# Kernel tuning notes

Hardware: AMD Instinct MI355X
Metric: run time of the kernel (lower is better)

Reference implementation:

```python
import jax, jax.numpy as jnp
import numpy as np

N_NODES = 100000
N_EDGES = 3200000
IN_CH, HID_CH, OUT_CH = 128, 64, 40


def gcn_conv(x, row, col, norm, W, b, n_nodes):
    # linear transform first (PyG GCNConv order), then normalized aggregation
    h = x @ W                                   # [N, out]
    msg = h[row] * norm[:, None]                # [E+N, out] gathered & scaled
    out = jax.ops.segment_sum(msg, col, num_segments=n_nodes)
    return out + b


def setup_inputs() -> dict:
    key = jax.random.key(0)
    k0, k1, k2, k3, k4, k5 = jax.random.split(key, 6)
    x = jax.random.normal(k0, (N_NODES, IN_CH), dtype=jnp.float32)
    edge_index = jax.random.randint(k1, (2, N_EDGES), 0, N_NODES, dtype=jnp.int64)
    # Glorot-ish init for weights
    W1 = jax.random.normal(k2, (IN_CH, HID_CH), dtype=jnp.float32) * (1.0 / np.sqrt(IN_CH))
    b1 = jnp.zeros((HID_CH,), dtype=jnp.float32)
    W2 = jax.random.normal(k3, (HID_CH, OUT_CH), dtype=jnp.float32) * (1.0 / np.sqrt(HID_CH))
    b2 = jnp.zeros((OUT_CH,), dtype=jnp.float32)
    return {"x": x, "edge_index": edge_index, "original_size": N_NODES,
            "W1": W1, "b1": b1, "W2": W2, "b2": b2}


def reference(x, edge_index, original_size, W1, b1, W2, b2):
    n = x.shape[0]
    # add self-loops (GCNConv default)
    loops = jnp.arange(n, dtype=edge_index.dtype)
    row = jnp.concatenate([edge_index[0], loops])   # source
    col = jnp.concatenate([edge_index[1], loops])   # target
    # symmetric normalization: deg over targets with unit edge weights
    deg = jax.ops.segment_sum(jnp.ones_like(col, dtype=x.dtype), col, num_segments=n)
    dinv = jnp.where(deg > 0, jax.lax.rsqrt(deg), 0.0)
    norm = dinv[row] * dinv[col]                    # [E+N]
    h = gcn_conv(x, row, col, norm, W1, b1, n)
    h = gcn_conv(h, row, col, norm, W2, b2, n)
    out = jax.nn.log_softmax(h, axis=1)
    return out[:original_size]
```

## Files before the change

### kernel.cpp

```cpp
#include <hip/hip_runtime.h>
#include <math.h>


#define NN 100000
#define NE 3200000
#define NBUK 391
#define BCAP 8704
#define EPB 16384
#define NBB ((NE + EPB - 1) / EPB)
#define NGB 782

typedef __attribute__((ext_vector_type(2))) float f32x2;


__device__ __forceinline__ unsigned bf16rne(float x) {
  unsigned u = __float_as_uint(x);
  return (u + 0x7fffu + ((u >> 16) & 1u)) >> 16;
}
__device__ __forceinline__ unsigned pack2(float lo, float hi) {
  return bf16rne(lo) | (bf16rne(hi) << 16);
}


__device__ __forceinline__ void pkfma(f32x2& a, f32x2 v, f32x2 f) {
  asm("v_pk_fma_f32 %0, %1, %2, %0" : "+v"(a) : "v"(v), "v"(f));
}

#define ACCP(vv, fp) {                                                      \
  f32x2 t0, t1, t2, t3;                                                     \
  t0.x = __uint_as_float((vv).x << 16);                                     \
  t0.y = __uint_as_float((vv).x & 0xffff0000u);                             \
  t1.x = __uint_as_float((vv).y << 16);                                     \
  t1.y = __uint_as_float((vv).y & 0xffff0000u);                             \
  t2.x = __uint_as_float((vv).z << 16);                                     \
  t2.y = __uint_as_float((vv).z & 0xffff0000u);                             \
  t3.x = __uint_as_float((vv).w << 16);                                     \
  t3.y = __uint_as_float((vv).w & 0xffff0000u);                             \
  pkfma(acc2[0], t0, fp);                                                   \
  pkfma(acc2[1], t1, fp);                                                   \
  pkfma(acc2[2], t2, fp);                                                   \
  pkfma(acc2[3], t3, fp);                                                   \
}


__global__ __launch_bounds__(256) void k_bucket_gemm1(const int* __restrict__ ei,
                                                      int* __restrict__ tail,
                                                      unsigned* __restrict__ bucket,
                                                      const float* __restrict__ x,
                                                      const float* __restrict__ W1,
                                                      unsigned* __restrict__ m1b) {
  __shared__ float smem[128 * 64 + 16 * 132];
  const int tid = threadIdx.x;
  const int bx = blockIdx.x;

  if (bx < NBB) {
    int* hist  = (int*)smem;
    int* wbase = hist + NBUK;
    int* loc   = wbase + NBUK;
    const int beg = bx * EPB;
    const int end = min(beg + EPB, NE);
    const int* col = ei + NE;
    for (int b = tid; b < NBUK; b += 256) { hist[b] = 0; loc[b] = 0; }
    __syncthreads();
    for (int e = beg + tid * 4; e < end; e += 1024) {
      int4 c4 = *(const int4*)(col + e);
      atomicAdd(&hist[c4.x >> 8], 1);
      atomicAdd(&hist[c4.y >> 8], 1);
      atomicAdd(&hist[c4.z >> 8], 1);
      atomicAdd(&hist[c4.w >> 8], 1);
    }
    __syncthreads();
    for (int b = tid; b < NBUK; b += 256)
      wbase[b] = atomicAdd(&tail[b], hist[b]);
    __syncthreads();
    for (int e = beg + tid * 4; e < end; e += 1024) {
      int4 c4 = *(const int4*)(col + e);
      int4 r4 = *(const int4*)(ei + e);
      {
        int b = c4.x >> 8;
        unsigned pos = (unsigned)(wbase[b] + atomicAdd(&loc[b], 1));
        if (pos < BCAP) bucket[(size_t)b * BCAP + pos] = ((unsigned)r4.x << 8) | (unsigned)(c4.x & 255);
      }
      {
        int b = c4.y >> 8;
        unsigned pos = (unsigned)(wbase[b] + atomicAdd(&loc[b], 1));
        if (pos < BCAP) bucket[(size_t)b * BCAP + pos] = ((unsigned)r4.y << 8) | (unsigned)(c4.y & 255);
      }
      {
        int b = c4.z >> 8;
        unsigned pos = (unsigned)(wbase[b] + atomicAdd(&loc[b], 1));
        if (pos < BCAP) bucket[(size_t)b * BCAP + pos] = ((unsigned)r4.z << 8) | (unsigned)(c4.z & 255);
      }
      {
        int b = c4.w >> 8;
        unsigned pos = (unsigned)(wbase[b] + atomicAdd(&loc[b], 1));
        if (pos < BCAP) bucket[(size_t)b * BCAP + pos] = ((unsigned)r4.w << 8) | (unsigned)(c4.w & 255);
      }
    }
    return;
  }

  float* ws = smem;
  float* xt = smem + 128 * 64;
  const int row0 = (bx - NBB) * 128;
  {
    const float4* __restrict__ w4 = (const float4*)W1;
    float4* __restrict__ s4 = (float4*)ws;
    for (int i = tid; i < 128 * 16; i += 256) s4[i] = w4[i];
  }
  const int cg = tid & 7;
  const int rg = tid >> 3;
  const int srow = tid & 127;
  const int skh = tid >> 7;
  float acc[4][8];
  #pragma unroll
  for (int i = 0; i < 4; ++i)
    #pragma unroll
    for (int j = 0; j < 8; ++j) acc[i][j] = 0.f;
  const float4* __restrict__ xt4 = (const float4*)xt;
  const float4* __restrict__ ws4 = (const float4*)ws;
  for (int ks = 0; ks < 8; ++ks) {
    __syncthreads();
    {
      int grow = row0 + srow; if (grow > NN - 1) grow = NN - 1;
      const float* xp = x + (size_t)grow * 128 + ks * 16 + skh * 8;
      float4 va = *(const float4*)xp;
      float4 vb = *(const float4*)(xp + 4);
      const int kb = skh * 8;
      xt[(kb + 0) * 132 + srow] = va.x;
      xt[(kb + 1) * 132 + srow] = va.y;
      xt[(kb + 2) * 132 + srow] = va.z;
      xt[(kb + 3) * 132 + srow] = va.w;
      xt[(kb + 4) * 132 + srow] = vb.x;
      xt[(kb + 5) * 132 + srow] = vb.y;
      xt[(kb + 6) * 132 + srow] = vb.z;
      xt[(kb + 7) * 132 + srow] = vb.w;
    }
    __syncthreads();
    #pragma unroll 4
    for (int kk = 0; kk < 16; ++kk) {
      const int k = ks * 16 + kk;
      float4 xv = xt4[kk * 33 + rg];
      float4 wa = ws4[k * 16 + cg * 2];
      float4 wb = ws4[k * 16 + cg * 2 + 1];
      float xr[4] = {xv.x, xv.y, xv.z, xv.w};
      float wc[8] = {wa.x, wa.y, wa.z, wa.w, wb.x, wb.y, wb.z, wb.w};
      #pragma unroll
      for (int i = 0; i < 4; ++i)
        #pragma unroll
        for (int j = 0; j < 8; ++j)
          acc[i][j] = fmaf(xr[i], wc[j], acc[i][j]);
    }
  }
  #pragma unroll
  for (int i = 0; i < 4; ++i) {
    const int row = row0 + rg * 4 + i;
    if (row < NN) {
      uint4 o;
      o.x = pack2(acc[i][0], acc[i][1]);
      o.y = pack2(acc[i][2], acc[i][3]);
      o.z = pack2(acc[i][4], acc[i][5]);
      o.w = pack2(acc[i][6], acc[i][7]);
      ((uint4*)m1b)[row * 8 + cg] = o;
    }
  }
}


__global__ __launch_bounds__(256) void k_sort(const unsigned* __restrict__ bucket,
                                              const int* __restrict__ tail,
                                              int* __restrict__ csr_src,
                                              int* __restrict__ offsets,
                                              float* __restrict__ dinv,
                                              unsigned* __restrict__ m1b) {
  __shared__ int h[256], base_[256], loc[256];
  __shared__ float dv[256];
  __shared__ int sorted[BCAP];
  __shared__ int wsum[4];
  __shared__ int seg0_s;
  const int b = blockIdx.x;
  const int lo = b << 8;
  const int nc = min(256, NN - lo);
  const int n = min(tail[b], BCAP);
  const unsigned* __restrict__ bk = bucket + (size_t)b * BCAP;
  const int tid = threadIdx.x, lane = tid & 63, wid = tid >> 6;
  h[tid] = 0; loc[tid] = 0;
  if (wid == 0) {
    int local = 0;
    const int lim = (b < NBUK) ? b : NBUK;
    for (int j = lane; j < lim; j += 64) local += min(tail[j], BCAP);
    #pragma unroll
    for (int d = 32; d > 0; d >>= 1) local += __shfl_xor(local, d, 64);
    if (lane == 0) seg0_s = local;
  }
  __syncthreads();
  const int seg0 = seg0_s;
  int i = tid * 4;
  for (; i + 3 < n; i += 1024) {
    uint4 v = *(const uint4*)(bk + i);
    atomicAdd(&h[v.x & 255u], 1);
    atomicAdd(&h[v.y & 255u], 1);
    atomicAdd(&h[v.z & 255u], 1);
    atomicAdd(&h[v.w & 255u], 1);
  }
  for (; i < n; ++i) atomicAdd(&h[bk[i] & 255u], 1);
  __syncthreads();
  {
    int v = h[tid];
    int s = v;
    #pragma unroll
    for (int d = 1; d < 64; d <<= 1) { int t = __shfl_up(s, d, 64); if (lane >= d) s += t; }
    if (lane == 63) wsum[wid] = s;
    __syncthreads();
    int wpre = 0;
    #pragma unroll
    for (int w = 0; w < 4; ++w) if (w < wid) wpre += wsum[w];
    int excl = wpre + s - v;
    base_[tid] = excl;
    const float dval = rsqrtf((float)(v + 1));
    dv[tid] = dval;
    if (tid < nc) {
      dinv[lo + tid] = dval;
      offsets[lo + tid] = seg0 + excl;
    }
  }
  if (b == NBUK - 1 && tid == 0) offsets[NN] = seg0 + n;
  __syncthreads();
  i = tid * 4;
  for (; i + 3 < n; i += 1024) {
    uint4 v = *(const uint4*)(bk + i);
    { int c = v.x & 255u; sorted[base_[c] + atomicAdd(&loc[c], 1)] = (int)(v.x >> 8); }
    { int c = v.y & 255u; sorted[base_[c] + atomicAdd(&loc[c], 1)] = (int)(v.y >> 8); }
    { int c = v.z & 255u; sorted[base_[c] + atomicAdd(&loc[c], 1)] = (int)(v.z >> 8); }
    { int c = v.w & 255u; sorted[base_[c] + atomicAdd(&loc[c], 1)] = (int)(v.w >> 8); }
  }
  for (; i < n; ++i) {
    unsigned ent = bk[i];
    int c = ent & 255u;
    sorted[base_[c] + atomicAdd(&loc[c], 1)] = (int)(ent >> 8);
  }
  __syncthreads();
  for (int t = tid; t < n; t += 256) csr_src[seg0 + t] = sorted[t];
  {
    const int q = tid & 7;
    uint4* __restrict__ m1rw = (uint4*)m1b;
    for (int r = tid >> 3; r < nc; r += 32) {
      const float d = dv[r];
      uint4 v = m1rw[(size_t)(lo + r) * 8 + q];
      v.x = pack2(__uint_as_float(v.x << 16) * d, __uint_as_float(v.x & 0xffff0000u) * d);
      v.y = pack2(__uint_as_float(v.y << 16) * d, __uint_as_float(v.y & 0xffff0000u) * d);
      v.z = pack2(__uint_as_float(v.z << 16) * d, __uint_as_float(v.z & 0xffff0000u) * d);
      v.w = pack2(__uint_as_float(v.w << 16) * d, __uint_as_float(v.w & 0xffff0000u) * d);
      m1rw[(size_t)(lo + r) * 8 + q] = v;
    }
  }
}


__global__ __launch_bounds__(256) void k_agg1(const unsigned* __restrict__ m1b,
                                              const int* __restrict__ offsets,
                                              const int* __restrict__ csr_src,
                                              const float* __restrict__ dinv,
                                              const float* __restrict__ b1,
                                              float* __restrict__ a1) {
  const int node = blockIdx.x * 4 + (threadIdx.x >> 6);
  const int lane = threadIdx.x & 63;
  const int e = lane >> 3;
  const int q = lane & 7;
  const uint4* __restrict__ m1v = (const uint4*)m1b;
  const int beg = offsets[node], end = offsets[node + 1];
  f32x2 acc2[4];
  #pragma unroll
  for (int j = 0; j < 4; ++j) { acc2[j].x = 0.f; acc2[j].y = 0.f; }
  for (int p = beg; p < end; p += 32) {
    const int i0 = p + e, i1 = p + 8 + e, i2 = p + 16 + e, i3 = p + 24 + e;
    const int s0 = csr_src[i0 < end ? i0 : beg];
    const int s1 = csr_src[i1 < end ? i1 : beg];
    const int s2 = csr_src[i2 < end ? i2 : beg];
    const int s3 = csr_src[i3 < end ? i3 : beg];
    f32x2 f0; f0.x = f0.y = (i0 < end) ? 1.f : 0.f;
    f32x2 f1; f1.x = f1.y = (i1 < end) ? 1.f : 0.f;
    f32x2 f2; f2.x = f2.y = (i2 < end) ? 1.f : 0.f;
    f32x2 f3; f3.x = f3.y = (i3 < end) ? 1.f : 0.f;
    uint4 v0 = m1v[s0 * 8 + q];
    uint4 v1 = m1v[s1 * 8 + q];
    uint4 v2 = m1v[s2 * 8 + q];
    uint4 v3 = m1v[s3 * 8 + q];
    ACCP(v0, f0);
    ACCP(v1, f1);
    ACCP(v2, f2);
    ACCP(v3, f3);
  }
  float acc[8];
  acc[0] = acc2[0].x; acc[1] = acc2[0].y; acc[2] = acc2[1].x; acc[3] = acc2[1].y;
  acc[4] = acc2[2].x; acc[5] = acc2[2].y; acc[6] = acc2[3].x; acc[7] = acc2[3].y;
  #pragma unroll
  for (int j = 0; j < 8; ++j) {
    acc[j] += __shfl_xor(acc[j], 8, 64);
    acc[j] += __shfl_xor(acc[j], 16, 64);
    acc[j] += __shfl_xor(acc[j], 32, 64);
  }
  if (e == 0) {
    uint4 sv = m1v[node * 8 + q];
    const float d = dinv[node];
    float4 bb0 = ((const float4*)b1)[q * 2];
    float4 bb1 = ((const float4*)b1)[q * 2 + 1];
    float4 o0, o1;
    o0.x = (acc[0] + __uint_as_float(sv.x << 16)) * d + bb0.x;
    o0.y = (acc[1] + __uint_as_float(sv.x & 0xffff0000u)) * d + bb0.y;
    o0.z = (acc[2] + __uint_as_float(sv.y << 16)) * d + bb0.z;
    o0.w = (acc[3] + __uint_as_float(sv.y & 0xffff0000u)) * d + bb0.w;
    o1.x = (acc[4] + __uint_as_float(sv.z << 16)) * d + bb1.x;
    o1.y = (acc[5] + __uint_as_float(sv.z & 0xffff0000u)) * d + bb1.y;
    o1.z = (acc[6] + __uint_as_float(sv.w << 16)) * d + bb1.z;
    o1.w = (acc[7] + __uint_as_float(sv.w & 0xffff0000u)) * d + bb1.w;
    ((float4*)a1)[node * 16 + q * 2] = o0;
    ((float4*)a1)[node * 16 + q * 2 + 1] = o1;
  }
}


__global__ __launch_bounds__(256) void k_gemm2(const float* __restrict__ a1,
                                               const float* __restrict__ W2,
                                               const float* __restrict__ dinv,
                                               unsigned* __restrict__ m2b) {
  __shared__ float ws[64 * 40];
  const int tid = threadIdx.x;
  for (int k = tid; k < 64 * 40; k += 256) ws[k] = W2[k];
  __syncthreads();
  const int idx = blockIdx.x * 256 + tid;
  if (idx >= NN * 20) return;
  const int node = idx / 20;
  const int c0 = (idx - node * 20) * 2;
  const float4* __restrict__ a4 = (const float4*)(a1 + node * 64);
  float acc0 = 0.f, acc1 = 0.f;
  #pragma unroll
  for (int k4 = 0; k4 < 16; ++k4) {
    float4 a = a4[k4];
    acc0 = fmaf(a.x, ws[(k4 * 4 + 0) * 40 + c0], acc0);
    acc1 = fmaf(a.x, ws[(k4 * 4 + 0) * 40 + c0 + 1], acc1);
    acc0 = fmaf(a.y, ws[(k4 * 4 + 1) * 40 + c0], acc0);
    acc1 = fmaf(a.y, ws[(k4 * 4 + 1) * 40 + c0 + 1], acc1);
    acc0 = fmaf(a.z, ws[(k4 * 4 + 2) * 40 + c0], acc0);
    acc1 = fmaf(a.z, ws[(k4 * 4 + 2) * 40 + c0 + 1], acc1);
    acc0 = fmaf(a.w, ws[(k4 * 4 + 3) * 40 + c0], acc0);
    acc1 = fmaf(a.w, ws[(k4 * 4 + 3) * 40 + c0 + 1], acc1);
  }
  const float d = dinv[node];
  m2b[idx] = pack2(acc0 * d, acc1 * d);
}


__device__ __forceinline__ float shfl1(float v, int src) {
  return __shfl(v, src & 63, 64);
}

__global__ __launch_bounds__(256) void k_agg2(const unsigned* __restrict__ m2b,
                                              const int* __restrict__ offsets,
                                              const int* __restrict__ csr_src,
                                              const float* __restrict__ dinv,
                                              const float* __restrict__ b2,
                                              float* __restrict__ out) {
  const int node = blockIdx.x * 4 + (threadIdx.x >> 6);
  const int lane = threadIdx.x & 63;
  const bool act = lane < 60;
  const int e = act ? (lane / 5) : 0;
  const int q = act ? (lane - e * 5) : 0;
  const uint4* __restrict__ m2v = (const uint4*)m2b;
  const int beg = offsets[node], end = offsets[node + 1];
  f32x2 acc2[4];
  #pragma unroll
  for (int j = 0; j < 4; ++j) { acc2[j].x = 0.f; acc2[j].y = 0.f; }
  for (int p = beg; p < end; p += 48) {
    const int i0 = p + e, i1 = p + 12 + e, i2 = p + 24 + e, i3 = p + 36 + e;
    const int s0 = csr_src[i0 < end ? i0 : beg];
    const int s1 = csr_src[i1 < end ? i1 : beg];
    const int s2 = csr_src[i2 < end ? i2 : beg];
    const int s3 = csr_src[i3 < end ? i3 : beg];
    f32x2 f0; f0.x = f0.y = (act && i0 < end) ? 1.f : 0.f;
    f32x2 f1; f1.x = f1.y = (act && i1 < end) ? 1.f : 0.f;
    f32x2 f2; f2.x = f2.y = (act && i2 < end) ? 1.f : 0.f;
    f32x2 f3; f3.x = f3.y = (act && i3 < end) ? 1.f : 0.f;
    uint4 v0 = m2v[s0 * 5 + q];
    uint4 v1 = m2v[s1 * 5 + q];
    uint4 v2 = m2v[s2 * 5 + q];
    uint4 v3 = m2v[s3 * 5 + q];
    ACCP(v0, f0);
    ACCP(v1, f1);
    ACCP(v2, f2);
    ACCP(v3, f3);
  }
  float acc[8];
  acc[0] = acc2[0].x; acc[1] = acc2[0].y; acc[2] = acc2[1].x; acc[3] = acc2[1].y;
  acc[4] = acc2[2].x; acc[5] = acc2[2].y; acc[6] = acc2[3].x; acc[7] = acc2[3].y;
  #pragma unroll
  for (int j = 0; j < 8; ++j) acc[j] += shfl1(acc[j], lane + 30);
  #pragma unroll
  for (int j = 0; j < 8; ++j) acc[j] += shfl1(acc[j], lane + 15);
  #pragma unroll
  for (int j = 0; j < 8; ++j) {
    float t1 = shfl1(acc[j], lane + 5);
    float t2 = shfl1(acc[j], lane + 10);
    acc[j] += t1 + t2;
  }
  const bool lead = (lane < 5);
  float r[8];
  #pragma unroll
  for (int j = 0; j < 8; ++j) r[j] = 0.f;
  if (lead) {
    uint4 sv = m2v[node * 5 + lane];
    const float d = dinv[node];
    float4 bb0 = ((const float4*)b2)[lane * 2];
    float4 bb1 = ((const float4*)b2)[lane * 2 + 1];
    r[0] = (acc[0] + __uint_as_float(sv.x << 16)) * d + bb0.x;
    r[1] = (acc[1] + __uint_as_float(sv.x & 0xffff0000u)) * d + bb0.y;
    r[2] = (acc[2] + __uint_as_float(sv.y << 16)) * d + bb0.z;
    r[3] = (acc[3] + __uint_as_float(sv.y & 0xffff0000u)) * d + bb0.w;
    r[4] = (acc[4] + __uint_as_float(sv.z << 16)) * d + bb1.x;
    r[5] = (acc[5] + __uint_as_float(sv.z & 0xffff0000u)) * d + bb1.y;
    r[6] = (acc[6] + __uint_as_float(sv.w << 16)) * d + bb1.z;
    r[7] = (acc[7] + __uint_as_float(sv.w & 0xffff0000u)) * d + bb1.w;
  }
  float mx = -INFINITY;
  if (lead) {
    mx = fmaxf(fmaxf(fmaxf(r[0], r[1]), fmaxf(r[2], r[3])),
               fmaxf(fmaxf(r[4], r[5]), fmaxf(r[6], r[7])));
  }
  #pragma unroll
  for (int d = 4; d > 0; d >>= 1) mx = fmaxf(mx, __shfl_xor(mx, d, 8));
  float se = 0.f;
  if (lead) {
    se = __expf(r[0] - mx) + __expf(r[1] - mx) + __expf(r[2] - mx) +
         __expf(r[3] - mx) + __expf(r[4] - mx) + __expf(r[5] - mx) +
         __expf(r[6] - mx) + __expf(r[7] - mx);
  }
  #pragma unroll
  for (int d = 4; d > 0; d >>= 1) se += __shfl_xor(se, d, 8);
  if (lead) {
    const float lse = mx + logf(se);
    float4 o0, o1;
    o0.x = r[0] - lse; o0.y = r[1] - lse; o0.z = r[2] - lse; o0.w = r[3] - lse;
    o1.x = r[4] - lse; o1.y = r[5] - lse; o1.z = r[6] - lse; o1.w = r[7] - lse;
    ((float4*)out)[node * 10 + lane * 2] = o0;
    ((float4*)out)[node * 10 + lane * 2 + 1] = o1;
  }
}


extern "C" void kernel_launch(void* const* d_in, const int* in_sizes, int n_in,
                              void* d_out, int out_size, void* d_ws, size_t ws_size,
                              hipStream_t stream) {
  const float* x   = (const float*)d_in[0];
  const int*   ei  = (const int*)d_in[1];
  const float* W1  = (const float*)d_in[3];
  const float* b1  = (const float*)d_in[4];
  const float* W2  = (const float*)d_in[5];
  const float* b2  = (const float*)d_in[6];
  float*       out = (float*)d_out;

  char* ws = (char*)d_ws;
  int*      tail    = (int*)(ws + 0);
  int*      offsets = (int*)(ws + (size_t)8 * 1024);
  float*    dinv    = (float*)(ws + (size_t)512 * 1024);
  int*      csr_src = (int*)(ws + (size_t)1536 * 1024);
  unsigned* m1b     = (unsigned*)(ws + (size_t)14848 * 1024);
  unsigned* bucket  = (unsigned*)(ws + (size_t)28160 * 1024);
  float*    a1      = (float*)(ws + (size_t)28160 * 1024);
  unsigned* m2b     = m1b;

  hipMemsetAsync(tail, 0, NBUK * 4, stream);
  k_bucket_gemm1<<<NBB + NGB, 256, 0, stream>>>(ei, tail, bucket, x, W1, m1b);
  k_sort<<<NBUK, 256, 0, stream>>>(bucket, tail, csr_src, offsets, dinv, m1b);
  k_agg1<<<NN / 4, 256, 0, stream>>>(m1b, offsets, csr_src, dinv, b1, a1);
  k_gemm2<<<(NN * 20 + 255) / 256, 256, 0, stream>>>(a1, W2, dinv, m2b);
  k_agg2<<<NN / 4, 256, 0, stream>>>(m2b, offsets, csr_src, dinv, b2, out);
}
```

Before: 202.4 us.

## Stage bucket scatter through LDS local sort for coalesced global writes

The edge-bucketing blocks now split their edge chunk into two halves of 8192. Each half is counting-sorted into shared memory using a block prefix scan over bucket histograms, then written to the global buckets as contiguous per-bucket runs, one wavefront per bucket. This replaces scattered single-word global stores with mostly contiguous writes. The cost is extra LDS traffic, more barriers, and twice as many global tail atomics.

```diff
diff --git a/kernel.cpp b/kernel.cpp
--- a/kernel.cpp
+++ b/kernel.cpp
@@ -7,6 +7,7 @@
 #define NBUK 391
 #define BCAP 8704
 #define EPB 16384
+#define SPE 8192
 #define NBB ((NE + EPB - 1) / EPB)
 #define NGB 782
 
@@ -52,50 +53,96 @@
   __shared__ float smem[128 * 64 + 16 * 132];
   const int tid = threadIdx.x;
   const int bx = blockIdx.x;
+  const int lane = tid & 63, wid = tid >> 6;
 
   if (bx < NBB) {
-    int* hist  = (int*)smem;
-    int* wbase = hist + NBUK;
+    int* ib = (int*)smem;
+    unsigned* sorted_l = (unsigned*)ib;
+    int* hist  = ib + SPE;
+    int* base_ = hist + NBUK;
+    int* wbase = base_ + NBUK;
     int* loc   = wbase + NBUK;
+    int* wsum  = loc + NBUK;
+    int* tot   = wsum + 4;
     const int beg = bx * EPB;
     const int end = min(beg + EPB, NE);
     const int* col = ei + NE;
-    for (int b = tid; b < NBUK; b += 256) { hist[b] = 0; loc[b] = 0; }
-    __syncthreads();
-    for (int e = beg + tid * 4; e < end; e += 1024) {
-      int4 c4 = *(const int4*)(col + e);
-      atomicAdd(&hist[c4.x >> 8], 1);
-      atomicAdd(&hist[c4.y >> 8], 1);
-      atomicAdd(&hist[c4.z >> 8], 1);
-      atomicAdd(&hist[c4.w >> 8], 1);
-    }
-    __syncthreads();
-    for (int b = tid; b < NBUK; b += 256)
-      wbase[b] = atomicAdd(&tail[b], hist[b]);
-    __syncthreads();
-    for (int e = beg + tid * 4; e < end; e += 1024) {
-      int4 c4 = *(const int4*)(col + e);
-      int4 r4 = *(const int4*)(ei + e);
+    for (int sp = 0; sp < 2; ++sp) {
+      const int sbeg = beg + sp * SPE;
+      const int send = min(sbeg + SPE, end);
+      if (sbeg >= send) break;
+      for (int b = tid; b < NBUK; b += 256) { hist[b] = 0; loc[b] = 0; }
+      __syncthreads();
+      for (int e = sbeg + tid * 4; e < send; e += 1024) {
+        int4 c4 = *(const int4*)(col + e);
+        atomicAdd(&hist[c4.x >> 8], 1);
+        atomicAdd(&hist[c4.y >> 8], 1);
+        atomicAdd(&hist[c4.z >> 8], 1);
+        atomicAdd(&hist[c4.w >> 8], 1);
+      }
+      __syncthreads();
       {
-        int b = c4.x >> 8;
-        unsigned pos = (unsigned)(wbase[b] + atomicAdd(&loc[b], 1));
-        if (pos < BCAP) bucket[(size_t)b * BCAP + pos] = ((unsigned)r4.x << 8) | (unsigned)(c4.x & 255);
+        int v = hist[tid];
+        int s = v;
+        #pragma unroll
+        for (int d = 1; d < 64; d <<= 1) { int t = __shfl_up(s, d, 64); if (lane >= d) s += t; }
+        if (lane == 63) wsum[wid] = s;
+        __syncthreads();
+        int wpre = 0;
+        #pragma unroll
+        for (int w = 0; w < 4; ++w) if (w < wid) wpre += wsum[w];
+        base_[tid] = wpre + s - v;
+        if (tid == 255) tot[0] = wpre + s;
+        __syncthreads();
+        int v2 = (tid < NBUK - 256) ? hist[256 + tid] : 0;
+        int s2 = v2;
+        #pragma unroll
+        for (int d = 1; d < 64; d <<= 1) { int t = __shfl_up(s2, d, 64); if (lane >= d) s2 += t; }
+        if (lane == 63) wsum[wid] = s2;
+        __syncthreads();
+        int wpre2 = 0;
+        #pragma unroll
+        for (int w = 0; w < 4; ++w) if (w < wid) wpre2 += wsum[w];
+        if (tid < NBUK - 256) base_[256 + tid] = tot[0] + wpre2 + s2 - v2;
       }
-      {
-        int b = c4.y >> 8;
-        unsigned pos = (unsigned)(wbase[b] + atomicAdd(&loc[b], 1));
-        if (pos < BCAP) bucket[(size_t)b * BCAP + pos] = ((unsigned)r4.y << 8) | (unsigned)(c4.y & 255);
+      for (int b = tid; b < NBUK; b += 256) wbase[b] = atomicAdd(&tail[b], hist[b]);
+      __syncthreads();
+      for (int e = sbeg + tid * 4; e < send; e += 1024) {
+        int4 c4 = *(const int4*)(col + e);
+        int4 r4 = *(const int4*)(ei + e);
+        {
+          int b = c4.x >> 8;
+          int p = base_[b] + atomicAdd(&loc[b], 1);
+          sorted_l[p] = ((unsigned)r4.x << 8) | (unsigned)(c4.x & 255);
+        }
+        {
+          int b = c4.y >> 8;
+          int p = base_[b] + atomicAdd(&loc[b], 1);
+          sorted_l[p] = ((unsigned)r4.y << 8) | (unsigned)(c4.y & 255);
+        }
+        {
+          int b = c4.z >> 8;
+          int p = base_[b] + atomicAdd(&loc[b], 1);
+          sorted_l[p] = ((unsigned)r4.z << 8) | (unsigned)(c4.z & 255);
+        }
+        {
+          int b = c4.w >> 8;
+          int p = base_[b] + atomicAdd(&loc[b], 1);
+          sorted_l[p] = ((unsigned)r4.w << 8) | (unsigned)(c4.w & 255);
+        }
       }
-      {
-        int b = c4.z >> 8;
-        unsigned pos = (unsigned)(wbase[b] + atomicAdd(&loc[b], 1));
-        if (pos < BCAP) bucket[(size_t)b * BCAP + pos] = ((unsigned)r4.z << 8) | (unsigned)(c4.z & 255);
+      __syncthreads();
+      for (int b = wid; b < NBUK; b += 4) {
+        const int cnt = hist[b];
+        const int gb = wbase[b];
+        const int lb = base_[b];
+        unsigned* dst = bucket + (size_t)b * BCAP;
+        for (int i = lane; i < cnt; i += 64) {
+          unsigned pos = (unsigned)(gb + i);
+          if (pos < BCAP) dst[pos] = sorted_l[lb + i];
+        }
       }
-      {
-        int b = c4.w >> 8;
-        unsigned pos = (unsigned)(wbase[b] + atomicAdd(&loc[b], 1));
-        if (pos < BCAP) bucket[(size_t)b * BCAP + pos] = ((unsigned)r4.w << 8) | (unsigned)(c4.w & 255);
-      }
+      __syncthreads();
     }
     return;
   }
```

New measurement: 221.3 us. 1.09x slower.

## Fuse second-layer GEMM into first aggregation kernel via wave shuffles

Applied to the files above, without the earlier changes.

Folds the layer-2 linear transform into k_agg1. Each wave computes its node's 64-wide aggregated row, then broadcasts those values with shuffles and dots them against W2 held in shared memory, writing dinv-scaled bf16 messages directly. This removes the fp32 a1 intermediate round trip through global memory and one kernel launch. In exchange, every agg1 block now loads W2 into LDS and each wave performs 64 shuffles plus FMAs, with 24 lanes doing no useful work.

```diff
diff --git a/kernel.cpp b/kernel.cpp
--- a/kernel.cpp
+++ b/kernel.cpp
@@ -40,6 +40,10 @@
   pkfma(acc2[1], t1, fp);                                                   \
   pkfma(acc2[2], t2, fp);                                                   \
   pkfma(acc2[3], t3, fp);                                                   \
+}
+
+__device__ __forceinline__ float shfl1(float v, int src) {
+  return __shfl(v, src & 63, 64);
 }
 
 
@@ -262,9 +266,14 @@
                                               const int* __restrict__ csr_src,
                                               const float* __restrict__ dinv,
                                               const float* __restrict__ b1,
-                                              float* __restrict__ a1) {
-  const int node = blockIdx.x * 4 + (threadIdx.x >> 6);
-  const int lane = threadIdx.x & 63;
+                                              const float* __restrict__ W2,
+                                              unsigned* __restrict__ m2b) {
+  __shared__ float ws2[64 * 40];
+  const int tid = threadIdx.x;
+  for (int i = tid; i < 64 * 40; i += 256) ws2[i] = W2[i];
+  __syncthreads();
+  const int node = blockIdx.x * 4 + (tid >> 6);
+  const int lane = tid & 63;
   const int e = lane >> 3;
   const int q = lane & 7;
   const uint4* __restrict__ m1v = (const uint4*)m1b;
@@ -300,60 +309,35 @@
     acc[j] += __shfl_xor(acc[j], 16, 64);
     acc[j] += __shfl_xor(acc[j], 32, 64);
   }
-  if (e == 0) {
+  const float d = dinv[node];
+  float av[8];
+  {
     uint4 sv = m1v[node * 8 + q];
-    const float d = dinv[node];
     float4 bb0 = ((const float4*)b1)[q * 2];
     float4 bb1 = ((const float4*)b1)[q * 2 + 1];
-    float4 o0, o1;
-    o0.x = (acc[0] + __uint_as_float(sv.x << 16)) * d + bb0.x;
-    o0.y = (acc[1] + __uint_as_float(sv.x & 0xffff0000u)) * d + bb0.y;
-    o0.z = (acc[2] + __uint_as_float(sv.y << 16)) * d + bb0.z;
-    o0.w = (acc[3] + __uint_as_float(sv.y & 0xffff0000u)) * d + bb0.w;
-    o1.x = (acc[4] + __uint_as_float(sv.z << 16)) * d + bb1.x;
-    o1.y = (acc[5] + __uint_as_float(sv.z & 0xffff0000u)) * d + bb1.y;
-    o1.z = (acc[6] + __uint_as_float(sv.w << 16)) * d + bb1.z;
-    o1.w = (acc[7] + __uint_as_float(sv.w & 0xffff0000u)) * d + bb1.w;
-    ((float4*)a1)[node * 16 + q * 2] = o0;
-    ((float4*)a1)[node * 16 + q * 2 + 1] = o1;
-  }
-}
-
-
-__global__ __launch_bounds__(256) void k_gemm2(const float* __restrict__ a1,
-                                               const float* __restrict__ W2,
-                                               const float* __restrict__ dinv,
-                                               unsigned* __restrict__ m2b) {
-  __shared__ float ws[64 * 40];
-  const int tid = threadIdx.x;
-  for (int k = tid; k < 64 * 40; k += 256) ws[k] = W2[k];
-  __syncthreads();
-  const int idx = blockIdx.x * 256 + tid;
-  if (idx >= NN * 20) return;
-  const int node = idx / 20;
-  const int c0 = (idx - node * 20) * 2;
-  const float4* __restrict__ a4 = (const float4*)(a1 + node * 64);
-  float acc0 = 0.f, acc1 = 0.f;
-  #pragma unroll
-  for (int k4 = 0; k4 < 16; ++k4) {
-    float4 a = a4[k4];
-    acc0 = fmaf(a.x, ws[(k4 * 4 + 0) * 40 + c0], acc0);
-    acc1 = fmaf(a.x, ws[(k4 * 4 + 0) * 40 + c0 + 1], acc1);
-    acc0 = fmaf(a.y, ws[(k4 * 4 + 1) * 40 + c0], acc0);
-    acc1 = fmaf(a.y, ws[(k4 * 4 + 1) * 40 + c0 + 1], acc1);
-    acc0 = fmaf(a.z, ws[(k4 * 4 + 2) * 40 + c0], acc0);
-    acc1 = fmaf(a.z, ws[(k4 * 4 + 2) * 40 + c0 + 1], acc1);
-    acc0 = fmaf(a.w, ws[(k4 * 4 + 3) * 40 + c0], acc0);
-    acc1 = fmaf(a.w, ws[(k4 * 4 + 3) * 40 + c0 + 1], acc1);
-  }
-  const float d = dinv[node];
-  m2b[idx] = pack2(acc0 * d, acc1 * d);
-}
-
-
-__device__ __forceinline__ float shfl1(float v, int src) {
-  return __shfl(v, src & 63, 64);
-}
+    av[0] = (acc[0] + __uint_as_float(sv.x << 16)) * d + bb0.x;
+    av[1] = (acc[1] + __uint_as_float(sv.x & 0xffff0000u)) * d + bb0.y;
+    av[2] = (acc[2] + __uint_as_float(sv.y << 16)) * d + bb0.z;
+    av[3] = (acc[3] + __uint_as_float(sv.y & 0xffff0000u)) * d + bb0.w;
+    av[4] = (acc[4] + __uint_as_float(sv.z << 16)) * d + bb1.x;
+    av[5] = (acc[5] + __uint_as_float(sv.z & 0xffff0000u)) * d + bb1.y;
+    av[6] = (acc[6] + __uint_as_float(sv.w << 16)) * d + bb1.z;
+    av[7] = (acc[7] + __uint_as_float(sv.w & 0xffff0000u)) * d + bb1.w;
+  }
+  const int c = lane;
+  const int cc = (c < 40) ? c : 0;
+  float dot = 0.f;
+  #pragma unroll
+  for (int k = 0; k < 64; ++k) {
+    float contrib = shfl1(av[k & 7], k >> 3);
+    dot = fmaf(contrib, ws2[k * 40 + cc], dot);
+  }
+  float hi = shfl1(dot, lane + 1);
+  if (c < 40 && !(c & 1)) {
+    m2b[node * 20 + (c >> 1)] = pack2(dot * d, hi * d);
+  }
+}
+
 
 __global__ __launch_bounds__(256) void k_agg2(const unsigned* __restrict__ m2b,
                                               const int* __restrict__ offsets,
@@ -465,13 +449,11 @@
   int*      csr_src = (int*)(ws + (size_t)1536 * 1024);
   unsigned* m1b     = (unsigned*)(ws + (size_t)14848 * 1024);
   unsigned* bucket  = (unsigned*)(ws + (size_t)28160 * 1024);
-  float*    a1      = (float*)(ws + (size_t)28160 * 1024);
-  unsigned* m2b     = m1b;
+  unsigned* m2b     = (unsigned*)(ws + (size_t)28160 * 1024);
 
   hipMemsetAsync(tail, 0, NBUK * 4, stream);
   k_bucket_gemm1<<<NBB + NGB, 256, 0, stream>>>(ei, tail, bucket, x, W1, m1b);
   k_sort<<<NBUK, 256, 0, stream>>>(bucket, tail, csr_src, offsets, dinv, m1b);
-  k_agg1<<<NN / 4, 256, 0, stream>>>(m1b, offsets, csr_src, dinv, b1, a1);
-  k_gemm2<<<(NN * 20 + 255) / 256, 256, 0, stream>>>(a1, W2, dinv, m2b);
+  k_agg1<<<NN / 4, 256, 0, stream>>>(m1b, offsets, csr_src, dinv, b1, W2, m2b);
   k_agg2<<<NN / 4, 256, 0, stream>>>(m2b, offsets, csr_src, dinv, b2, out);
 }
```

Result: slower. 253.8 us (+25.4%).
